# Optimization experiments

Hardware: AMD Instinct MI355X
Metric: run time of the kernel (lower is better)

The kernel has to match this reference:

```python
import jax, jax.numpy as jnp
import numpy as np

N = 32768      # number of nodes (joint candidates)
DIN = 128      # NODE_INPUT_DIM
H1 = 128       # OUTPUT_SIZES[0]
DOUT = 128     # OUTPUT_SIZES[-1] == output_dim
T = 17         # number of node types / expert MLPs


def setup_inputs() -> dict:
    key = jax.random.key(0)
    ks = jax.random.split(key, 6)
    x = jax.random.normal(ks[0], (N, DIN), dtype=jnp.float32)
    node_types = jax.random.randint(ks[1], (N,), 0, T)
    # Stacked per-type MLP parameters (17 independent Linear-ReLU-Linear MLPs).
    W1 = jax.random.normal(ks[2], (T, DIN, H1), dtype=jnp.float32) / np.float32(np.sqrt(DIN))
    b1 = jax.random.normal(ks[3], (T, H1), dtype=jnp.float32) * 0.01
    W2 = jax.random.normal(ks[4], (T, H1, DOUT), dtype=jnp.float32) / np.float32(np.sqrt(H1))
    b2 = jax.random.normal(ks[5], (T, DOUT), dtype=jnp.float32) * 0.01
    return {"x": x, "W1": W1, "b1": b1, "W2": W2, "b2": b2, "node_types": node_types}


def reference(x, W1, b1, W2, b2, node_types):
    # Dense hard-routing: evaluate all 17 type-specific MLPs on every node,
    # then select each node's own type. Mathematically identical to the
    # boolean-mask gather/scatter loop in the torch module (each row of the
    # output is MLP_{node_types[n]}(x[n])), but fully vectorized and jittable.
    h = jax.nn.relu(jnp.einsum('nd,tdh->nth', x, W1) + b1)   # [N, T, H1]
    y = jnp.einsum('nth,thm->ntm', h, W2) + b2               # [N, T, DOUT]
    # gather the row matching each node's type (combine step)
    out = jnp.take_along_axis(y, node_types[:, None, None], axis=1)[:, 0, :]  # [N, DOUT]
    return out
```

## Files before the change

kernel.cpp:

```cpp
#include <hip/hip_runtime.h>

#define N_NODES 32768
#define NB 128
#define DIM 128
#define NT 17
#define ROWS 64
#define BPT 48
#define LP 136

typedef short bf16x8 __attribute__((ext_vector_type(8)));
typedef float f32x4 __attribute__((ext_vector_type(4)));

#define WS_OFFSETS   0
#define WS_BLOCKHIST 128
#define WS_BLOCKBASE 8960
#define WS_LRANK     17664
#define WS_PERM      50432
#define WS_W1T       181504
#define WS_W2T       738560

__device__ __forceinline__ unsigned short f2bf(float f) {
  unsigned int u = __float_as_uint(f);
  u += 0x7FFFu + ((u >> 16) & 1u);
  return (unsigned short)(u >> 16);
}

__global__ void k_pre(const int* __restrict__ types, int* __restrict__ blockHist,
                      unsigned char* __restrict__ lrank,
                      const float* __restrict__ W1, const float* __restrict__ W2,
                      unsigned short* __restrict__ W1t, unsigned short* __restrict__ W2t) {
  int tid = threadIdx.x;
  if (blockIdx.x < NB) {
    __shared__ int h[NT];
    if (tid < NT) h[tid] = 0;
    __syncthreads();
    int i = blockIdx.x * 256 + tid;
    int r = atomicAdd(&h[types[i]], 1);
    lrank[i] = (unsigned char)r;
    __syncthreads();
    if (tid < NT) blockHist[blockIdx.x * NT + tid] = h[tid];
    return;
  }
  int m = blockIdx.x - NB;
  const float* src = (m < NT) ? (W1 + (size_t)m * DIM * DIM)
                              : (W2 + (size_t)(m - NT) * DIM * DIM);
  unsigned short* dst = (m < NT) ? (W1t + (size_t)m * DIM * DIM)
                                 : (W2t + (size_t)(m - NT) * DIM * DIM);
  __shared__ unsigned short tile[DIM * LP];
  #pragma unroll
  for (int it = 0; it < 32; ++it) {
    int s = tid + it * 256;
    int n = s & 127, kp = s >> 7;
    float a = src[(size_t)(2 * kp) * DIM + n];
    float b = src[(size_t)(2 * kp + 1) * DIM + n];
    unsigned int pk = (unsigned int)f2bf(a) | ((unsigned int)f2bf(b) << 16);
    *(unsigned int*)&tile[n * LP + 2 * kp] = pk;
  }
  __syncthreads();
  #pragma unroll
  for (int it = 0; it < 8; ++it) {
    int s = tid + it * 256;
    int n = s >> 4, c = s & 15;
    *(uint4*)(dst + (size_t)n * DIM + c * 8) = *(const uint4*)&tile[n * LP + c * 8];
  }
}

__global__ void k_scan(const int* __restrict__ blockHist, int* __restrict__ blockBase,
                       int* __restrict__ offsets) {
  __shared__ int sh[NB * NT];
  __shared__ int soff[NT + 1];
  int tid = threadIdx.x;
  for (int s = tid; s < NB * NT; s += 256) sh[s] = blockHist[s];
  __syncthreads();
  if (tid < NT) {
    int acc = 0;
    for (int b = 0; b < NB; ++b) { int v = sh[b * NT + tid]; sh[b * NT + tid] = acc; acc += v; }
    soff[tid] = acc;
  }
  __syncthreads();
  if (tid == 0) {
    int acc = 0;
    for (int t = 0; t < NT; ++t) { int c = soff[t]; soff[t] = acc; acc += c; }
    soff[NT] = acc;
  }
  __syncthreads();
  if (tid < NT + 1) offsets[tid] = soff[tid];
  for (int s = tid; s < NB * NT; s += 256) {
    int t = s % NT;
    blockBase[s] = sh[s] + soff[t];
  }
}

__global__ void k_scatter(const int* __restrict__ types, const unsigned char* __restrict__ lrank,
                          const int* __restrict__ blockBase, int* __restrict__ perm) {
  __shared__ int bb[NT];
  int tid = threadIdx.x;
  if (tid < NT) bb[tid] = blockBase[blockIdx.x * NT + tid];
  __syncthreads();
  int i = blockIdx.x * 256 + tid;
  perm[bb[types[i]] + lrank[i]] = i;
}

__global__ __launch_bounds__(256, 2)
void k_mlp(const float* __restrict__ x, const float* __restrict__ b1,
           const float* __restrict__ b2, float* __restrict__ out,
           const int* __restrict__ offsets, const int* __restrict__ perm,
           const unsigned short* __restrict__ W1t, const unsigned short* __restrict__ W2t) {
  int t = blockIdx.y;
  int seg_start = offsets[t], seg_end = offsets[t + 1];
  int row_start = seg_start + blockIdx.x * ROWS;
  if (row_start >= seg_end) return;

  __shared__ unsigned short Xs[ROWS * LP];
  __shared__ unsigned short Ws[DIM * LP];
  __shared__ int prow[ROWS];

  int tid = threadIdx.x;
  if (tid < ROWS) {
    int idx = row_start + tid;
    if (idx >= seg_end) idx = seg_start;
    prow[tid] = perm[idx];
  }
  __syncthreads();

  #pragma unroll
  for (int it = 0; it < 8; ++it) {
    int s = tid + it * 256;
    int r = s >> 5, c4 = s & 31;
    const float4 v = *(const float4*)(x + (size_t)prow[r] * DIM + c4 * 4);
    unsigned int lo = (unsigned int)f2bf(v.x) | ((unsigned int)f2bf(v.y) << 16);
    unsigned int hi = (unsigned int)f2bf(v.z) | ((unsigned int)f2bf(v.w) << 16);
    *(uint2*)&Xs[r * LP + c4 * 4] = make_uint2(lo, hi);
  }
  const unsigned short* w1g = W1t + (size_t)t * DIM * DIM;
  #pragma unroll
  for (int it = 0; it < 8; ++it) {
    int s = tid + it * 256;
    int n = s >> 4, c = s & 15;
    *(uint4*)&Ws[n * LP + c * 8] = *(const uint4*)(w1g + n * DIM + c * 8);
  }
  __syncthreads();

  int lane = tid & 63, w = tid >> 6;
  int l15 = lane & 15, q = lane >> 4;
  int arow = w * 16 + l15;
  int kb = q * 8;

  f32x4 acc[8];
  #pragma unroll
  for (int nt = 0; nt < 8; ++nt) acc[nt] = (f32x4){0.f, 0.f, 0.f, 0.f};
  #pragma unroll
  for (int kk = 0; kk < 4; ++kk) {
    bf16x8 a = *(const bf16x8*)&Xs[arow * LP + kk * 32 + kb];
    #pragma unroll
    for (int nt = 0; nt < 8; ++nt) {
      bf16x8 b = *(const bf16x8*)&Ws[(nt * 16 + l15) * LP + kk * 32 + kb];
      acc[nt] = __builtin_amdgcn_mfma_f32_16x16x32_bf16(a, b, acc[nt], 0, 0, 0);
    }
  }
  const float* b1t = b1 + t * DIM;
  #pragma unroll
  for (int nt = 0; nt < 8; ++nt) {
    int col = nt * 16 + l15;
    float bias = b1t[col];
    #pragma unroll
    for (int r = 0; r < 4; ++r) {
      int row = w * 16 + q * 4 + r;
      Xs[row * LP + col] = f2bf(fmaxf(acc[nt][r] + bias, 0.f));
    }
  }
  __syncthreads();

  const unsigned short* w2g = W2t + (size_t)t * DIM * DIM;
  #pragma unroll
  for (int it = 0; it < 8; ++it) {
    int s = tid + it * 256;
    int n = s >> 4, c = s & 15;
    *(uint4*)&Ws[n * LP + c * 8] = *(const uint4*)(w2g + n * DIM + c * 8);
  }
  __syncthreads();

  #pragma unroll
  for (int nt = 0; nt < 8; ++nt) acc[nt] = (f32x4){0.f, 0.f, 0.f, 0.f};
  #pragma unroll
  for (int kk = 0; kk < 4; ++kk) {
    bf16x8 a = *(const bf16x8*)&Xs[arow * LP + kk * 32 + kb];
    #pragma unroll
    for (int nt = 0; nt < 8; ++nt) {
      bf16x8 b = *(const bf16x8*)&Ws[(nt * 16 + l15) * LP + kk * 32 + kb];
      acc[nt] = __builtin_amdgcn_mfma_f32_16x16x32_bf16(a, b, acc[nt], 0, 0, 0);
    }
  }
  const float* b2t = b2 + t * DIM;
  int r0 = w * 16 + q * 4;
  int gr[4]; bool vld[4];
  #pragma unroll
  for (int r = 0; r < 4; ++r) {
    vld[r] = (row_start + r0 + r) < seg_end;
    gr[r] = prow[r0 + r];
  }
  #pragma unroll
  for (int nt = 0; nt < 8; ++nt) {
    int col = nt * 16 + l15;
    float bias = b2t[col];
    #pragma unroll
    for (int r = 0; r < 4; ++r) {
      if (vld[r]) out[(size_t)gr[r] * DIM + col] = acc[nt][r] + bias;
    }
  }
}

extern "C" void kernel_launch(void* const* d_in, const int* in_sizes, int n_in,
                              void* d_out, int out_size, void* d_ws, size_t ws_size,
                              hipStream_t stream) {
  const float* x  = (const float*)d_in[0];
  const float* W1 = (const float*)d_in[1];
  const float* b1 = (const float*)d_in[2];
  const float* W2 = (const float*)d_in[3];
  const float* b2 = (const float*)d_in[4];
  const int* types = (const int*)d_in[5];
  float* out = (float*)d_out;

  char* ws = (char*)d_ws;
  int* offsets = (int*)(ws + WS_OFFSETS);
  int* blockHist = (int*)(ws + WS_BLOCKHIST);
  int* blockBase = (int*)(ws + WS_BLOCKBASE);
  unsigned char* lrank = (unsigned char*)(ws + WS_LRANK);
  int* perm    = (int*)(ws + WS_PERM);
  unsigned short* W1t = (unsigned short*)(ws + WS_W1T);
  unsigned short* W2t = (unsigned short*)(ws + WS_W2T);

  k_pre<<<NB + 2 * NT, 256, 0, stream>>>(types, blockHist, lrank, W1, W2, W1t, W2t);
  k_scan<<<1, 256, 0, stream>>>(blockHist, blockBase, offsets);
  k_scatter<<<NB, 256, 0, stream>>>(types, lrank, blockBase, perm);
  dim3 grid(BPT, NT);
  k_mlp<<<grid, 256, 0, stream>>>(x, b1, b2, out, offsets, perm, W1t, W2t);
}
```

Before: 99.09 us.

## Fuse scan and scatter into MLP kernel via per-block histogram search

Removes the separate scan and scatter kernels. Each MLP block now computes a prefix sum over the per-block type histograms for its expert and scans the packed type/rank array to build its own row list. This cuts two kernel launches and their serial dependencies, and the launch bound is raised to 3 blocks per CU. The cost is redundant scan work and extra reads of the type array in every MLP block.

Result: faster. 94.65 us (-4.5%).

```diff
diff --git a/kernel.cpp b/kernel.cpp
--- a/kernel.cpp
+++ b/kernel.cpp
@@ -11,13 +11,10 @@
 typedef short bf16x8 __attribute__((ext_vector_type(8)));
 typedef float f32x4 __attribute__((ext_vector_type(4)));
 
-#define WS_OFFSETS   0
-#define WS_BLOCKHIST 128
-#define WS_BLOCKBASE 8960
-#define WS_LRANK     17664
-#define WS_PERM      50432
-#define WS_W1T       181504
-#define WS_W2T       738560
+#define WS_BLOCKHIST 0
+#define WS_TL        8704
+#define WS_W1T       74240
+#define WS_W2T       631296
 
 __device__ __forceinline__ unsigned short f2bf(float f) {
   unsigned int u = __float_as_uint(f);
@@ -26,7 +23,7 @@
 }
 
 __global__ void k_pre(const int* __restrict__ types, int* __restrict__ blockHist,
-                      unsigned char* __restrict__ lrank,
+                      unsigned short* __restrict__ tl,
                       const float* __restrict__ W1, const float* __restrict__ W2,
                       unsigned short* __restrict__ W1t, unsigned short* __restrict__ W2t) {
   int tid = threadIdx.x;
@@ -35,8 +32,9 @@
     if (tid < NT) h[tid] = 0;
     __syncthreads();
     int i = blockIdx.x * 256 + tid;
-    int r = atomicAdd(&h[types[i]], 1);
-    lrank[i] = (unsigned char)r;
+    int ty = types[i];
+    int r = atomicAdd(&h[ty], 1);
+    tl[i] = (unsigned short)(ty | (r << 5));
     __syncthreads();
     if (tid < NT) blockHist[blockIdx.x * NT + tid] = h[tid];
     return;
@@ -65,61 +63,47 @@
   }
 }
 
-__global__ void k_scan(const int* __restrict__ blockHist, int* __restrict__ blockBase,
-                       int* __restrict__ offsets) {
-  __shared__ int sh[NB * NT];
-  __shared__ int soff[NT + 1];
-  int tid = threadIdx.x;
-  for (int s = tid; s < NB * NT; s += 256) sh[s] = blockHist[s];
-  __syncthreads();
-  if (tid < NT) {
-    int acc = 0;
-    for (int b = 0; b < NB; ++b) { int v = sh[b * NT + tid]; sh[b * NT + tid] = acc; acc += v; }
-    soff[tid] = acc;
-  }
-  __syncthreads();
-  if (tid == 0) {
-    int acc = 0;
-    for (int t = 0; t < NT; ++t) { int c = soff[t]; soff[t] = acc; acc += c; }
-    soff[NT] = acc;
-  }
-  __syncthreads();
-  if (tid < NT + 1) offsets[tid] = soff[tid];
-  for (int s = tid; s < NB * NT; s += 256) {
-    int t = s % NT;
-    blockBase[s] = sh[s] + soff[t];
-  }
-}
-
-__global__ void k_scatter(const int* __restrict__ types, const unsigned char* __restrict__ lrank,
-                          const int* __restrict__ blockBase, int* __restrict__ perm) {
-  __shared__ int bb[NT];
-  int tid = threadIdx.x;
-  if (tid < NT) bb[tid] = blockBase[blockIdx.x * NT + tid];
-  __syncthreads();
-  int i = blockIdx.x * 256 + tid;
-  perm[bb[types[i]] + lrank[i]] = i;
-}
-
-__global__ __launch_bounds__(256, 2)
+__global__ __launch_bounds__(256, 3)
 void k_mlp(const float* __restrict__ x, const float* __restrict__ b1,
            const float* __restrict__ b2, float* __restrict__ out,
-           const int* __restrict__ offsets, const int* __restrict__ perm,
+           const int* __restrict__ blockHist, const unsigned short* __restrict__ tl,
            const unsigned short* __restrict__ W1t, const unsigned short* __restrict__ W2t) {
   int t = blockIdx.y;
-  int seg_start = offsets[t], seg_end = offsets[t + 1];
-  int row_start = seg_start + blockIdx.x * ROWS;
-  if (row_start >= seg_end) return;
-
+  int tid = threadIdx.x;
+
+  __shared__ int cc[NB];
+  __shared__ int prow[ROWS];
   __shared__ unsigned short Xs[ROWS * LP];
   __shared__ unsigned short Ws[DIM * LP];
-  __shared__ int prow[ROWS];
-
-  int tid = threadIdx.x;
-  if (tid < ROWS) {
-    int idx = row_start + tid;
-    if (idx >= seg_end) idx = seg_start;
-    prow[tid] = perm[idx];
+
+  int v = 0;
+  if (tid < NB) { v = blockHist[tid * NT + t]; cc[tid] = v; }
+  #pragma unroll
+  for (int off = 1; off < NB; off <<= 1) {
+    __syncthreads();
+    int add = (tid < NB && tid >= off) ? cc[tid - off] : 0;
+    __syncthreads();
+    if (tid < NB) { v += add; cc[tid] = v; }
+  }
+  __syncthreads();
+  int total = cc[NB - 1];
+  int win_lo = blockIdx.x * ROWS;
+  if (win_lo >= total) return;
+  int win_hi = win_lo + ROWS;
+  int nvalid = min(ROWS, total - win_lo);
+
+  if (tid < ROWS) prow[tid] = 0;
+  __syncthreads();
+
+  int lo = 0, hi = NB;
+  while (lo < hi) { int mid = (lo + hi) >> 1; if (cc[mid] > win_lo) hi = mid; else lo = mid + 1; }
+  for (int b = lo; b < NB; ++b) {
+    int excl = b ? cc[b - 1] : 0;
+    if (excl >= win_hi) break;
+    unsigned short pv = tl[b * 256 + tid];
+    int ty = pv & 31, lr = pv >> 5;
+    int g = excl + lr;
+    if (ty == t && g >= win_lo && g < win_hi) prow[g - win_lo] = b * 256 + tid;
   }
   __syncthreads();
 
@@ -127,10 +111,11 @@
   for (int it = 0; it < 8; ++it) {
     int s = tid + it * 256;
     int r = s >> 5, c4 = s & 31;
-    const float4 v = *(const float4*)(x + (size_t)prow[r] * DIM + c4 * 4);
-    unsigned int lo = (unsigned int)f2bf(v.x) | ((unsigned int)f2bf(v.y) << 16);
-    unsigned int hi = (unsigned int)f2bf(v.z) | ((unsigned int)f2bf(v.w) << 16);
-    *(uint2*)&Xs[r * LP + c4 * 4] = make_uint2(lo, hi);
+    int rr = (r < nvalid) ? r : 0;
+    const float4 vx = *(const float4*)(x + (size_t)prow[rr] * DIM + c4 * 4);
+    unsigned int lo2 = (unsigned int)f2bf(vx.x) | ((unsigned int)f2bf(vx.y) << 16);
+    unsigned int hi2 = (unsigned int)f2bf(vx.z) | ((unsigned int)f2bf(vx.w) << 16);
+    *(uint2*)&Xs[r * LP + c4 * 4] = make_uint2(lo2, hi2);
   }
   const unsigned short* w1g = W1t + (size_t)t * DIM * DIM;
   #pragma unroll
@@ -196,7 +181,7 @@
   int gr[4]; bool vld[4];
   #pragma unroll
   for (int r = 0; r < 4; ++r) {
-    vld[r] = (row_start + r0 + r) < seg_end;
+    vld[r] = (r0 + r) < nvalid;
     gr[r] = prow[r0 + r];
   }
   #pragma unroll
@@ -222,17 +207,12 @@
   float* out = (float*)d_out;
 
   char* ws = (char*)d_ws;
-  int* offsets = (int*)(ws + WS_OFFSETS);
   int* blockHist = (int*)(ws + WS_BLOCKHIST);
-  int* blockBase = (int*)(ws + WS_BLOCKBASE);
-  unsigned char* lrank = (unsigned char*)(ws + WS_LRANK);
-  int* perm    = (int*)(ws + WS_PERM);
+  unsigned short* tl  = (unsigned short*)(ws + WS_TL);
   unsigned short* W1t = (unsigned short*)(ws + WS_W1T);
   unsigned short* W2t = (unsigned short*)(ws + WS_W2T);
 
-  k_pre<<<NB + 2 * NT, 256, 0, stream>>>(types, blockHist, lrank, W1, W2, W1t, W2t);
-  k_scan<<<1, 256, 0, stream>>>(blockHist, blockBase, offsets);
-  k_scatter<<<NB, 256, 0, stream>>>(types, lrank, blockBase, perm);
+  k_pre<<<NB + 2 * NT, 256, 0, stream>>>(types, blockHist, tl, W1, W2, W1t, W2t);
   dim3 grid(BPT, NT);
-  k_mlp<<<grid, 256, 0, stream>>>(x, b1, b2, out, offsets, perm, W1t, W2t);
-}
+  k_mlp<<<grid, 256, 0, stream>>>(x, b1, b2, out, blockHist, tl, W1t, W2t);
+}
```
